# Optimization experiments

Hardware: AMD Instinct MI355X
Metric: run time of the kernel (lower is better)

The kernel has to match this reference:

```python
import jax, jax.numpy as jnp
import numpy as np
import math

EMB = 512

def setup_inputs() -> dict:
    key = jax.random.key(0)
    ks = jax.random.split(key, 7)
    B, L, E = 4, 4096, EMB
    s = 1.0 / math.sqrt(E)
    return {
        "x": jax.random.normal(ks[0], (B, L, E), dtype=jnp.float32),
        "Wq": jax.random.normal(ks[1], (E, E), dtype=jnp.float32) * s,
        "bq": jax.random.normal(ks[2], (E,), dtype=jnp.float32) * 0.01,
        "Wk": jax.random.normal(ks[3], (E, E), dtype=jnp.float32) * s,
        "bk": jax.random.normal(ks[4], (E,), dtype=jnp.float32) * 0.01,
        "Wv": jax.random.normal(ks[5], (E, E), dtype=jnp.float32) * s,
        "bv": jax.random.normal(ks[6], (E,), dtype=jnp.float32) * 0.01,
    }

def reference(x, Wq, bq, Wk, bk, Wv, bv):
    # x: [B, L, E]; Linear weights stored torch-style [out, in]
    E = x.shape[-1]
    L = x.shape[1]
    q = jnp.einsum('ble,fe->blf', x, Wq) + bq
    k = jnp.einsum('ble,fe->blf', x, Wk) + bk
    v = jnp.einsum('ble,fe->blf', x, Wv) + bv
    qk = jnp.einsum('bqe,bke->bqk', q, k)  # [B, L, L]
    # causal mask: strict upper triangle filled with -1e9 BEFORE scaling (as in source)
    mask = jnp.triu(jnp.ones((L, L), dtype=bool), k=1)
    qk = jnp.where(mask, jnp.float32(-1e9), qk)
    att = jax.nn.softmax(qk / jnp.sqrt(jnp.float32(E)), axis=-1)
    return jnp.einsum('bqk,bke->bqe', att, v)
```

## Files before the change

kernel.cpp:

```cpp
#include <hip/hip_runtime.h>

typedef unsigned short u16;
typedef unsigned int u32;
typedef short bf16x8 __attribute__((ext_vector_type(8)));
typedef float f32x4 __attribute__((ext_vector_type(4)));
typedef u16 u16x8 __attribute__((ext_vector_type(8)));
typedef u16 u16x4 __attribute__((ext_vector_type(4)));

typedef const __attribute__((address_space(1))) u32* gas_ptr;
typedef __attribute__((address_space(3))) u32* las_ptr;

#define LQ   4096
#define EMB  512
#define NB   4
#define MROWS (NB * LQ)
#define QSCALE 0.04419417382415922f

__device__ __forceinline__ u16 f2bf(float f) {
  unsigned u = __builtin_bit_cast(unsigned, f);
  u += 0x7fffu + ((u >> 16) & 1u);
  return (u16)(u >> 16);
}
__device__ __forceinline__ float bf2f(u16 h) {
  unsigned u = ((unsigned)h) << 16;
  return __builtin_bit_cast(float, u);
}

__global__ void prep_w(const float* __restrict__ Wq, const float* __restrict__ bq,
                       const float* __restrict__ Wk, const float* __restrict__ bk,
                       const float* __restrict__ Wv, const float* __restrict__ bv,
                       u16* __restrict__ wqb, u16* __restrict__ wkb, u16* __restrict__ wvb,
                       float* __restrict__ bias) {
  int i = blockIdx.x * 256 + threadIdx.x;
  if (i < EMB * EMB) {
    wqb[i] = f2bf(Wq[i] * QSCALE);
    wkb[i] = f2bf(Wk[i]);
    wvb[i] = f2bf(Wv[i]);
  }
  if (i < EMB) {
    bias[i]           = bq[i] * QSCALE;
    bias[EMB + i]     = bk[i];
    bias[2 * EMB + i] = bv[i];
  }
}

__global__ void prep_x(const float* __restrict__ x, u16* __restrict__ xb) {
  int i = blockIdx.x * 256 + threadIdx.x;
  const float4* p = (const float4*)(x + (size_t)i * 8);
  float4 a = p[0], b = p[1];
  u16x8 o;
  o[0] = f2bf(a.x); o[1] = f2bf(a.y); o[2] = f2bf(a.z); o[3] = f2bf(a.w);
  o[4] = f2bf(b.x); o[5] = f2bf(b.y); o[6] = f2bf(b.z); o[7] = f2bf(b.w);
  *(u16x8*)(xb + (size_t)i * 8) = o;
}

__device__ __forceinline__ void stage128_256t(const u16* g, int ld, u16* lds, int tid) {
  int wave = tid >> 6;
#pragma unroll
  for (int p = 0; p < 4; ++p) {
    int c = tid + p * 256;
    int row = c >> 3, hh = c & 7;
    int h = hh ^ (row & 7);
    const u16* src = g + (size_t)row * ld + h * 8;
    u16* dst = lds + wave * 512 + p * 2048;
    __builtin_amdgcn_global_load_lds((gas_ptr)(const void*)src, (las_ptr)(void*)dst, 16, 0, 0);
  }
}

__device__ __forceinline__ void gemm_core_db(
    const u16* __restrict__ A, int lda,
    const u16* __restrict__ B, int ldb,
    int kIters, u16* lds,
    f32x4 acc[4][4], int tid, int lane, int wr, int wc)
{
  stage128_256t(A, lda, lds, tid);
  stage128_256t(B, ldb, lds + 8192, tid);
  for (int kb = 0; kb < kIters; ++kb) {
    u16* ldsA = lds + (kb & 1) * 16384;
    u16* ldsB = ldsA + 8192;
    __syncthreads();
    if (kb + 1 < kIters) {
      u16* nA = lds + ((kb + 1) & 1) * 16384;
      stage128_256t(A + (kb + 1) * 64, lda, nA, tid);
      stage128_256t(B + (kb + 1) * 64, ldb, nA + 8192, tid);
    }
#pragma unroll
    for (int s = 0; s < 2; ++s) {
      bf16x8 af[4], bfr[4];
#pragma unroll
      for (int m = 0; m < 4; ++m) {
        int row = wr * 64 + m * 16 + (lane & 15);
        int hh = (s * 4 + (lane >> 4)) ^ (row & 7);
        af[m] = *(const bf16x8*)(ldsA + row * 64 + hh * 8);
      }
#pragma unroll
      for (int n = 0; n < 4; ++n) {
        int row = wc * 64 + n * 16 + (lane & 15);
        int hh = (s * 4 + (lane >> 4)) ^ (row & 7);
        bfr[n] = *(const bf16x8*)(ldsB + row * 64 + hh * 8);
      }
#pragma unroll
      for (int m = 0; m < 4; ++m)
#pragma unroll
        for (int n = 0; n < 4; ++n)
          acc[m][n] = __builtin_amdgcn_mfma_f32_16x16x32_bf16(af[m], bfr[n], acc[m][n], 0, 0, 0);
    }
  }
}

__global__ __launch_bounds__(256, 2) void k_qkv(
    const u16* __restrict__ xb,
    const u16* __restrict__ w0, const u16* __restrict__ w1, const u16* __restrict__ w2,
    const float* __restrict__ bias,
    u16* __restrict__ o0, u16* __restrict__ o1, u16* __restrict__ o2)
{
  __shared__ __align__(16) u16 lds[32768];
  int bi = blockIdx.x;
  int which = bi >> 9;
  int t = bi & 511;
  int rt = t >> 2, ct = t & 3;
  const u16* W = (which == 0) ? w0 : (which == 1) ? w1 : w2;
  const float* bs = bias + which * EMB;
  int tid = threadIdx.x, lane = tid & 63, wave = tid >> 6;
  int wr = wave >> 1, wc = wave & 1;
  f32x4 acc[4][4];
#pragma unroll
  for (int m = 0; m < 4; ++m)
#pragma unroll
    for (int n = 0; n < 4; ++n) acc[m][n] = (f32x4)0.0f;

  gemm_core_db(xb + (size_t)rt * 128 * EMB, EMB,
               W + (size_t)ct * 128 * EMB, EMB, EMB / 64,
               lds, acc, tid, lane, wr, wc);

#pragma unroll
  for (int m = 0; m < 4; ++m)
#pragma unroll
    for (int n = 0; n < 4; ++n) {
      int row0 = rt * 128 + wr * 64 + m * 16 + ((lane >> 4) << 2);
      int col  = ct * 128 + wc * 64 + n * 16 + (lane & 15);
      float bv = bs[col];
      if (which < 2) {
        u16* out = (which == 0) ? o0 : o1;
#pragma unroll
        for (int r = 0; r < 4; ++r)
          out[(size_t)(row0 + r) * EMB + col] = f2bf(acc[m][n][r] + bv);
      } else {
        int b = row0 >> 12, l0 = row0 & (LQ - 1);
        u16x4 pk;
#pragma unroll
        for (int r = 0; r < 4; ++r) pk[r] = f2bf(acc[m][n][r] + bv);
        *(u16x4*)(o2 + ((size_t)(b * EMB + col)) * LQ + l0) = pk;
      }
    }
}

__global__ __launch_bounds__(256, 2) void k_qk(
    const u16* __restrict__ Q, const u16* __restrict__ K,
    u16* __restrict__ S, int bstart)
{
  __shared__ __align__(16) u16 lds[32768];
  int t = blockIdx.x;
  int b_local = t / 528;
  int i = t - b_local * 528;
  int qi = (int)((sqrtf(8.f * (float)i + 1.f) - 1.f) * 0.5f);
  while ((qi + 1) * (qi + 2) / 2 <= i) ++qi;
  while (qi * (qi + 1) / 2 > i) --qi;
  int ki = i - qi * (qi + 1) / 2;
  int bg = bstart + b_local;

  int tid = threadIdx.x, lane = tid & 63, wave = tid >> 6;
  int wr = wave >> 1, wc = wave & 1;
  f32x4 acc[4][4];
#pragma unroll
  for (int m = 0; m < 4; ++m)
#pragma unroll
    for (int n = 0; n < 4; ++n) acc[m][n] = (f32x4)0.0f;

  gemm_core_db(Q + ((size_t)bg * LQ + qi * 128) * EMB, EMB,
               K + ((size_t)bg * LQ + ki * 128) * EMB, EMB, EMB / 64,
               lds, acc, tid, lane, wr, wc);

  u16* Sb = S + (size_t)b_local * LQ * LQ;
#pragma unroll
  for (int m = 0; m < 4; ++m)
#pragma unroll
    for (int n = 0; n < 4; ++n) {
      int row0 = qi * 128 + wr * 64 + m * 16 + ((lane >> 4) << 2);
      int col  = ki * 128 + wc * 64 + n * 16 + (lane & 15);
#pragma unroll
      for (int r = 0; r < 4; ++r) {
        int row = row0 + r;
        float v = (col > row) ? -1e9f : acc[m][n][r];
        Sb[(size_t)row * LQ + col] = f2bf(v);
      }
    }
}

__global__ __launch_bounds__(512, 1) void k_pv2(
    const u16* __restrict__ S, const u16* __restrict__ Vt,
    float* __restrict__ out, int bstart, int bcount)
{
  __shared__ __align__(16) u16 sA[4096];
  __shared__ __align__(16) u16 sB[65536];
  __shared__ __align__(16) u16 sP[2048];
  __shared__ float sF[32];
  __shared__ float sL[32];

  int bi = blockIdx.x;
  int pairidx = bi / bcount;
  int b_local = bi - pairidx * bcount;
  int bg = bstart + b_local;
  int rtA = pairidx, rtB = 127 - pairidx;
  int unitsA = (rtA + 2) >> 1;
  int total = unitsA + ((rtB + 2) >> 1);

  const u16* Sbase = S + (size_t)b_local * LQ * LQ;
  const u16* Vb = Vt + (size_t)bg * EMB * LQ;

  int tid = threadIdx.x, lane = tid & 63, wave = tid >> 6;
  int l15 = lane & 15, lhi = lane >> 4;
  int srow = tid >> 4;
  int scg  = tid & 15;
  int shh  = ((scg >> 1) ^ (srow & 7)) * 8 + (scg & 1) * 4;

  f32x4 acc[2][4];
#pragma unroll
  for (int m = 0; m < 2; ++m)
#pragma unroll
    for (int n = 0; n < 4; ++n) acc[m][n] = (f32x4)0.0f;
  float mrun = -3.0e38f, lrun = 0.f;

  auto stage_unit = [&](int i) {
    int ph = (i >= unitsA) ? 1 : 0;
    int rt = ph ? rtB : rtA;
    int k0 = (ph ? (i - unitsA) : i) * 64;
    const u16* ga = Sbase + (size_t)(rt * 32) * LQ + k0;
    const u16* gb = Vb + k0;
    u16* bA = sA + (i & 1) * 2048;
    u16* bB = sB + (i & 1) * 32768;
    if (wave < 4) {
      int ca = wave * 64 + lane;
      int row = ca >> 3, h = ca & 7;
      __builtin_amdgcn_global_load_lds(
          (gas_ptr)(const void*)(ga + (size_t)row * LQ + (h ^ (row & 7)) * 8),
          (las_ptr)(void*)(bA + wave * 512), 16, 0, 0);
    }
#pragma unroll
    for (int p = 0; p < 8; ++p) {
      int cb = wave * 512 + p * 64 + lane;
      int col = cb >> 3, h = cb & 7;
      __builtin_amdgcn_global_load_lds(
          (gas_ptr)(const void*)(gb + (size_t)col * LQ + (h ^ (col & 7)) * 8),
          (las_ptr)(void*)(bB + wave * 4096 + p * 512), 16, 0, 0);
    }
  };

  auto epilogue = [&](int rt) {
    if (scg == 0) sL[srow] = 1.0f / lrun;
    __syncthreads();
    float li[2][4];
#pragma unroll
    for (int m = 0; m < 2; ++m)
#pragma unroll
      for (int r = 0; r < 4; ++r) li[m][r] = sL[m * 16 + lhi * 4 + r];
#pragma unroll
    for (int m = 0; m < 2; ++m)
#pragma unroll
      for (int r = 0; r < 4; ++r) {
        int grow = rt * 32 + m * 16 + lhi * 4 + r;
#pragma unroll
        for (int n = 0; n < 4; ++n) {
          int col = wave * 64 + n * 16 + l15;
          out[((size_t)bg * LQ + grow) * EMB + col] = acc[m][n][r] * li[m][r];
        }
      }
#pragma unroll
    for (int m = 0; m < 2; ++m)
#pragma unroll
      for (int n = 0; n < 4; ++n) acc[m][n] = (f32x4)0.0f;
    mrun = -3.0e38f;
    lrun = 0.f;
  };

  stage_unit(0);

  for (int i = 0; i < total; ++i) {
    u16* bA = sA + (i & 1) * 2048;
    u16* bB = sB + (i & 1) * 32768;
    __syncthreads();
    if (i + 1 < total) stage_unit(i + 1);
    if (i == unitsA) epilogue(rtA);

    u16x4 raw = *(const u16x4*)(bA + srow * 64 + shh);
    float s0 = bf2f(raw[0]), s1 = bf2f(raw[1]), s2 = bf2f(raw[2]), s3 = bf2f(raw[3]);
    float tmax = fmaxf(fmaxf(s0, s1), fmaxf(s2, s3));
#pragma unroll
    for (int off = 1; off <= 8; off <<= 1) tmax = fmaxf(tmax, __shfl_xor(tmax, off));
    float mnew = (tmax > mrun + 8.f) ? tmax : mrun;
    float f = __expf(mrun - mnew);
    mrun = mnew;
    float e0 = __expf(s0 - mrun), e1 = __expf(s1 - mrun);
    float e2 = __expf(s2 - mrun), e3 = __expf(s3 - mrun);
    float rs = (e0 + e1) + (e2 + e3);
#pragma unroll
    for (int off = 1; off <= 8; off <<= 1) rs += __shfl_xor(rs, off);
    lrun = lrun * f + rs;
    u16x4 pk;
    pk[0] = f2bf(e0); pk[1] = f2bf(e1); pk[2] = f2bf(e2); pk[3] = f2bf(e3);
    *(u16x4*)(sP + srow * 64 + shh) = pk;
    if (scg == 0) sF[srow] = f;
    __syncthreads();

    float fr[2][4];
#pragma unroll
    for (int m = 0; m < 2; ++m)
#pragma unroll
      for (int r = 0; r < 4; ++r) fr[m][r] = sF[m * 16 + lhi * 4 + r];
#pragma unroll
    for (int m = 0; m < 2; ++m)
#pragma unroll
      for (int n = 0; n < 4; ++n)
#pragma unroll
        for (int r = 0; r < 4; ++r) acc[m][n][r] *= fr[m][r];

#pragma unroll
    for (int s = 0; s < 2; ++s) {
      bf16x8 af[2];
#pragma unroll
      for (int m = 0; m < 2; ++m) {
        int row = m * 16 + l15;
        int hh = (s * 4 + lhi) ^ (row & 7);
        af[m] = *(const bf16x8*)(sP + row * 64 + hh * 8);
      }
#pragma unroll
      for (int n = 0; n < 4; ++n) {
        int col = wave * 64 + n * 16 + l15;
        int hh = (s * 4 + lhi) ^ (col & 7);
        bf16x8 bv = *(const bf16x8*)(bB + col * 64 + hh * 8);
#pragma unroll
        for (int m = 0; m < 2; ++m)
          acc[m][n] = __builtin_amdgcn_mfma_f32_16x16x32_bf16(af[m], bv, acc[m][n], 0, 0, 0);
      }
    }
  }
  __syncthreads();
  epilogue(rtB);
}

extern "C" void kernel_launch(void* const* d_in, const int* in_sizes, int n_in,
                              void* d_out, int out_size, void* d_ws, size_t ws_size,
                              hipStream_t stream) {
  const float* x  = (const float*)d_in[0];
  const float* Wq = (const float*)d_in[1];
  const float* bq = (const float*)d_in[2];
  const float* Wk = (const float*)d_in[3];
  const float* bk = (const float*)d_in[4];
  const float* Wv = (const float*)d_in[5];
  const float* bv = (const float*)d_in[6];

  char* ws = (char*)d_ws;
  size_t off = 0;
  u16* xb  = (u16*)(ws + off); off += (size_t)MROWS * EMB * 2;
  u16* wqb = (u16*)(ws + off); off += (size_t)EMB * EMB * 2;
  u16* wkb = (u16*)(ws + off); off += (size_t)EMB * EMB * 2;
  u16* wvb = (u16*)(ws + off); off += (size_t)EMB * EMB * 2;
  float* bias = (float*)(ws + off); off += 3 * EMB * 4;
  off = (off + 255) & ~(size_t)255;
  u16* Qb  = (u16*)(ws + off); off += (size_t)MROWS * EMB * 2;
  u16* Kb  = (u16*)(ws + off); off += (size_t)MROWS * EMB * 2;
  u16* Vtb = (u16*)(ws + off); off += (size_t)MROWS * EMB * 2;
  size_t fixed = off;
  size_t s_full = (size_t)NB * LQ * LQ * 2;
  int bcap = (ws_size >= fixed + s_full) ? NB : 1;
  u16* Sb = (u16*)(ws + fixed);

  prep_w<<<(EMB * EMB + 255) / 256, 256, 0, stream>>>(Wq, bq, Wk, bk, Wv, bv,
                                                      wqb, wkb, wvb, bias);
  prep_x<<<(MROWS * EMB / 8) / 256, 256, 0, stream>>>(x, xb);

  k_qkv<<<1536, 256, 0, stream>>>(xb, wqb, wkb, wvb, bias, Qb, Kb, Vtb);

  for (int bs = 0; bs < NB; bs += bcap) {
    int bc = (bs + bcap <= NB) ? bcap : (NB - bs);
    k_qk<<<528 * bc, 256, 0, stream>>>(Qb, Kb, Sb, bs);
    k_pv2<<<64 * bc, 512, 0, stream>>>(Sb, Vtb, (float*)d_out, bs, bc);
  }
}
```

Measured before the change: 244.4 us.

## Restructure PV kernel to 128-row tiles with pipelined register softmax

Replaces the paired 32-row PV kernel with one that handles a 128-row query tile per block. Each V tile staged in LDS is now reused across 128 rows instead of 32. S rows are loaded into registers two steps ahead, and the softmax for the next step is computed while the current step's MFMAs run. Accumulator rescaling is skipped when no row's running max changed. The cost is fewer blocks (32 per batch) with uneven causal work per block, which risks load imbalance and lower occupancy from a large accumulator register footprint.

```diff
diff --git a/kernel.cpp b/kernel.cpp
--- a/kernel.cpp
+++ b/kernel.cpp
@@ -197,155 +197,172 @@
     }
 }
 
-__global__ __launch_bounds__(512, 1) void k_pv2(
+__global__ __launch_bounds__(512, 1) void k_pv3(
     const u16* __restrict__ S, const u16* __restrict__ Vt,
     float* __restrict__ out, int bstart, int bcount)
 {
-  __shared__ __align__(16) u16 sA[4096];
-  __shared__ __align__(16) u16 sB[65536];
-  __shared__ __align__(16) u16 sP[2048];
-  __shared__ float sF[32];
-  __shared__ float sL[32];
+  __shared__ __align__(16) u16 sV[65536];
+  __shared__ __align__(16) u16 sP[8192];
+  __shared__ float sF[128];
+  __shared__ float sL[128];
+  __shared__ int   sFlag[8];
 
   int bi = blockIdx.x;
-  int pairidx = bi / bcount;
-  int b_local = bi - pairidx * bcount;
+  int rt = bi / bcount;
+  int b_local = bi - rt * bcount;
   int bg = bstart + b_local;
-  int rtA = pairidx, rtB = 127 - pairidx;
-  int unitsA = (rtA + 2) >> 1;
-  int total = unitsA + ((rtB + 2) >> 1);
-
-  const u16* Sbase = S + (size_t)b_local * LQ * LQ;
+  int total = 2 * (rt + 1);
+
+  const u16* Sbase = S + ((size_t)b_local * LQ + rt * 128) * LQ;
   const u16* Vb = Vt + (size_t)bg * EMB * LQ;
 
   int tid = threadIdx.x, lane = tid & 63, wave = tid >> 6;
   int l15 = lane & 15, lhi = lane >> 4;
-  int srow = tid >> 4;
-  int scg  = tid & 15;
-  int shh  = ((scg >> 1) ^ (srow & 7)) * 8 + (scg & 1) * 4;
-
-  f32x4 acc[2][4];
-#pragma unroll
-  for (int m = 0; m < 2; ++m)
+  int r0 = tid >> 3;
+  int cc = tid & 7;
+
+  f32x4 acc[8][4];
+#pragma unroll
+  for (int m = 0; m < 8; ++m)
 #pragma unroll
     for (int n = 0; n < 4; ++n) acc[m][n] = (f32x4)0.0f;
-  float mrun = -3.0e38f, lrun = 0.f;
-
-  auto stage_unit = [&](int i) {
-    int ph = (i >= unitsA) ? 1 : 0;
-    int rt = ph ? rtB : rtA;
-    int k0 = (ph ? (i - unitsA) : i) * 64;
-    const u16* ga = Sbase + (size_t)(rt * 32) * LQ + k0;
-    const u16* gb = Vb + k0;
-    u16* bA = sA + (i & 1) * 2048;
-    u16* bB = sB + (i & 1) * 32768;
-    if (wave < 4) {
-      int ca = wave * 64 + lane;
-      int row = ca >> 3, h = ca & 7;
-      __builtin_amdgcn_global_load_lds(
-          (gas_ptr)(const void*)(ga + (size_t)row * LQ + (h ^ (row & 7)) * 8),
-          (las_ptr)(void*)(bA + wave * 512), 16, 0, 0);
-    }
+  float m0 = -3.0e38f, m1 = -3.0e38f, l0 = 0.f, l1 = 0.f;
+
+  auto stageV = [&](int i, u16* buf) {
+    const u16* gb = Vb + i * 64;
 #pragma unroll
     for (int p = 0; p < 8; ++p) {
       int cb = wave * 512 + p * 64 + lane;
-      int col = cb >> 3, h = cb & 7;
+      int col = cb >> 3, h = (cb & 7) ^ (col & 7);
       __builtin_amdgcn_global_load_lds(
-          (gas_ptr)(const void*)(gb + (size_t)col * LQ + (h ^ (col & 7)) * 8),
-          (las_ptr)(void*)(bB + wave * 4096 + p * 512), 16, 0, 0);
+          (gas_ptr)(const void*)(gb + (size_t)col * LQ + h * 8),
+          (las_ptr)(void*)(buf + wave * 4096 + p * 512), 16, 0, 0);
     }
   };
-
-  auto epilogue = [&](int rt) {
-    if (scg == 0) sL[srow] = 1.0f / lrun;
+  auto issueA = [&](int i, u16x8 (&ar)[2]) {
+    const u16* ga = Sbase + i * 64 + cc * 8;
+    ar[0] = *(const u16x8*)(ga + (size_t)r0 * LQ);
+    ar[1] = *(const u16x8*)(ga + (size_t)(r0 + 64) * LQ);
+  };
+  auto softmax = [&](u16x8 (&ar)[2], u16x8& pf0, u16x8& pf1, float& fo0, float& fo1) {
+    float s0[8], s1[8];
+#pragma unroll
+    for (int j = 0; j < 8; ++j) { s0[j] = bf2f(ar[0][j]); s1[j] = bf2f(ar[1][j]); }
+    float mx0 = fmaxf(fmaxf(fmaxf(s0[0], s0[1]), fmaxf(s0[2], s0[3])),
+                      fmaxf(fmaxf(s0[4], s0[5]), fmaxf(s0[6], s0[7])));
+    float mx1 = fmaxf(fmaxf(fmaxf(s1[0], s1[1]), fmaxf(s1[2], s1[3])),
+                      fmaxf(fmaxf(s1[4], s1[5]), fmaxf(s1[6], s1[7])));
+#pragma unroll
+    for (int off = 1; off <= 4; off <<= 1) {
+      mx0 = fmaxf(mx0, __shfl_xor(mx0, off));
+      mx1 = fmaxf(mx1, __shfl_xor(mx1, off));
+    }
+    float mn0 = (mx0 > m0 + 8.f) ? mx0 : m0;
+    float mn1 = (mx1 > m1 + 8.f) ? mx1 : m1;
+    float f0 = __expf(m0 - mn0);
+    float f1 = __expf(m1 - mn1);
+    m0 = mn0; m1 = mn1;
+    float t0 = 0.f, t1 = 0.f;
+#pragma unroll
+    for (int j = 0; j < 8; ++j) {
+      float e0 = __expf(s0[j] - m0);
+      float e1 = __expf(s1[j] - m1);
+      t0 += e0; t1 += e1;
+      pf0[j] = f2bf(e0); pf1[j] = f2bf(e1);
+    }
+#pragma unroll
+    for (int off = 1; off <= 4; off <<= 1) {
+      t0 += __shfl_xor(t0, off);
+      t1 += __shfl_xor(t1, off);
+    }
+    l0 = l0 * f0 + t0;
+    l1 = l1 * f1 + t1;
+    fo0 = f0; fo1 = f1;
+  };
+
+  u16x8 ar0[2], ar1[2];
+  issueA(0, ar0);
+  stageV(0, sV);
+  issueA(1, ar1);
+  {
+    u16x8 pf0, pf1; float f0s, f1s;
+    softmax(ar0, pf0, pf1, f0s, f1s);
+    int hh = cc ^ (r0 & 7);
+    *(u16x8*)(sP + r0 * 64 + hh * 8) = pf0;
+    *(u16x8*)(sP + (r0 + 64) * 64 + hh * 8) = pf1;
+    if (cc == 0) { sF[r0] = f0s; sF[r0 + 64] = f1s; }
+    int fl = __any((f0s < 1.f) || (f1s < 1.f)) ? 1 : 0;
+    if (lane == 0) sFlag[wave] = fl;
+  }
+
+  auto body = [&](int i, u16x8 (&cur)[2], u16x8 (&nxt)[2], u16* vb, u16* vbN) {
     __syncthreads();
-    float li[2][4];
-#pragma unroll
-    for (int m = 0; m < 2; ++m)
-#pragma unroll
-      for (int r = 0; r < 4; ++r) li[m][r] = sL[m * 16 + lhi * 4 + r];
-#pragma unroll
-    for (int m = 0; m < 2; ++m)
-#pragma unroll
-      for (int r = 0; r < 4; ++r) {
-        int grow = rt * 32 + m * 16 + lhi * 4 + r;
-#pragma unroll
-        for (int n = 0; n < 4; ++n) {
-          int col = wave * 64 + n * 16 + l15;
-          out[((size_t)bg * LQ + grow) * EMB + col] = acc[m][n][r] * li[m][r];
-        }
-      }
-#pragma unroll
-    for (int m = 0; m < 2; ++m)
-#pragma unroll
-      for (int n = 0; n < 4; ++n) acc[m][n] = (f32x4)0.0f;
-    mrun = -3.0e38f;
-    lrun = 0.f;
-  };
-
-  stage_unit(0);
-
-  for (int i = 0; i < total; ++i) {
-    u16* bA = sA + (i & 1) * 2048;
-    u16* bB = sB + (i & 1) * 32768;
-    __syncthreads();
-    if (i + 1 < total) stage_unit(i + 1);
-    if (i == unitsA) epilogue(rtA);
-
-    u16x4 raw = *(const u16x4*)(bA + srow * 64 + shh);
-    float s0 = bf2f(raw[0]), s1 = bf2f(raw[1]), s2 = bf2f(raw[2]), s3 = bf2f(raw[3]);
-    float tmax = fmaxf(fmaxf(s0, s1), fmaxf(s2, s3));
-#pragma unroll
-    for (int off = 1; off <= 8; off <<= 1) tmax = fmaxf(tmax, __shfl_xor(tmax, off));
-    float mnew = (tmax > mrun + 8.f) ? tmax : mrun;
-    float f = __expf(mrun - mnew);
-    mrun = mnew;
-    float e0 = __expf(s0 - mrun), e1 = __expf(s1 - mrun);
-    float e2 = __expf(s2 - mrun), e3 = __expf(s3 - mrun);
-    float rs = (e0 + e1) + (e2 + e3);
-#pragma unroll
-    for (int off = 1; off <= 8; off <<= 1) rs += __shfl_xor(rs, off);
-    lrun = lrun * f + rs;
-    u16x4 pk;
-    pk[0] = f2bf(e0); pk[1] = f2bf(e1); pk[2] = f2bf(e2); pk[3] = f2bf(e3);
-    *(u16x4*)(sP + srow * 64 + shh) = pk;
-    if (scg == 0) sF[srow] = f;
-    __syncthreads();
-
-    float fr[2][4];
-#pragma unroll
-    for (int m = 0; m < 2; ++m)
-#pragma unroll
-      for (int r = 0; r < 4; ++r) fr[m][r] = sF[m * 16 + lhi * 4 + r];
-#pragma unroll
-    for (int m = 0; m < 2; ++m)
-#pragma unroll
-      for (int n = 0; n < 4; ++n)
-#pragma unroll
-        for (int r = 0; r < 4; ++r) acc[m][n][r] *= fr[m][r];
-
+    bool have = (i + 1 < total);
+    if (have) stageV(i + 1, vbN);
+    if (i + 2 < total) issueA(i + 2, cur);
+    int4 fA = *(const int4*)&sFlag[0];
+    int4 fB = *(const int4*)&sFlag[4];
+    if (fA.x | fA.y | fA.z | fA.w | fB.x | fB.y | fB.z | fB.w) {
+#pragma unroll
+      for (int m = 0; m < 8; ++m) {
+        f32x4 sf = *(const f32x4*)&sF[m * 16 + lhi * 4];
+#pragma unroll
+        for (int n = 0; n < 4; ++n)
+#pragma unroll
+          for (int r = 0; r < 4; ++r) acc[m][n][r] *= sf[r];
+      }
+    }
+    u16x8 pf0, pf1; float f0s = 1.f, f1s = 1.f;
+    if (have) softmax(nxt, pf0, pf1, f0s, f1s);
 #pragma unroll
     for (int s = 0; s < 2; ++s) {
-      bf16x8 af[2];
-#pragma unroll
-      for (int m = 0; m < 2; ++m) {
-        int row = m * 16 + l15;
-        int hh = (s * 4 + lhi) ^ (row & 7);
-        af[m] = *(const bf16x8*)(sP + row * 64 + hh * 8);
-      }
+      bf16x8 bv[4];
 #pragma unroll
       for (int n = 0; n < 4; ++n) {
         int col = wave * 64 + n * 16 + l15;
-        int hh = (s * 4 + lhi) ^ (col & 7);
-        bf16x8 bv = *(const bf16x8*)(bB + col * 64 + hh * 8);
-#pragma unroll
-        for (int m = 0; m < 2; ++m)
-          acc[m][n] = __builtin_amdgcn_mfma_f32_16x16x32_bf16(af[m], bv, acc[m][n], 0, 0, 0);
-      }
-    }
-  }
+        bv[n] = *(const bf16x8*)(vb + col * 64 + ((s * 4 + lhi) ^ (col & 7)) * 8);
+      }
+#pragma unroll
+      for (int m = 0; m < 8; ++m) {
+        int row = m * 16 + l15;
+        bf16x8 pa = *(const bf16x8*)(sP + row * 64 + ((s * 4 + lhi) ^ (row & 7)) * 8);
+#pragma unroll
+        for (int n = 0; n < 4; ++n)
+          acc[m][n] = __builtin_amdgcn_mfma_f32_16x16x32_bf16(pa, bv[n], acc[m][n], 0, 0, 0);
+      }
+    }
+    __syncthreads();
+    if (have) {
+      int hh = cc ^ (r0 & 7);
+      *(u16x8*)(sP + r0 * 64 + hh * 8) = pf0;
+      *(u16x8*)(sP + (r0 + 64) * 64 + hh * 8) = pf1;
+      if (cc == 0) { sF[r0] = f0s; sF[r0 + 64] = f1s; }
+      int fl = __any((f0s < 1.f) || (f1s < 1.f)) ? 1 : 0;
+      if (lane == 0) sFlag[wave] = fl;
+    }
+  };
+
+  int half = total >> 1;
+  for (int h = 0; h < half; ++h) {
+    body(2 * h,     ar0, ar1, sV,         sV + 32768);
+    body(2 * h + 1, ar1, ar0, sV + 32768, sV);
+  }
+
+  if (cc == 0) { sL[r0] = 1.0f / l0; sL[r0 + 64] = 1.0f / l1; }
   __syncthreads();
-  epilogue(rtB);
+#pragma unroll
+  for (int m = 0; m < 8; ++m) {
+    f32x4 li = *(const f32x4*)&sL[m * 16 + lhi * 4];
+#pragma unroll
+    for (int r = 0; r < 4; ++r) {
+      int grow = rt * 128 + m * 16 + lhi * 4 + r;
+#pragma unroll
+      for (int n = 0; n < 4; ++n) {
+        int col = wave * 64 + n * 16 + l15;
+        out[((size_t)bg * LQ + grow) * EMB + col] = acc[m][n][r] * li[r];
+      }
+    }
+  }
 }
 
 extern "C" void kernel_launch(void* const* d_in, const int* in_sizes, int n_in,
@@ -384,6 +401,6 @@
   for (int bs = 0; bs < NB; bs += bcap) {
     int bc = (bs + bcap <= NB) ? bcap : (NB - bs);
     k_qk<<<528 * bc, 256, 0, stream>>>(Qb, Kb, Sb, bs);
-    k_pv2<<<64 * bc, 512, 0, stream>>>(Sb, Vtb, (float*)d_out, bs, bc);
-  }
-}
+    k_pv3<<<32 * bc, 512, 0, stream>>>(Sb, Vtb, (float*)d_out, bs, bc);
+  }
+}
```

Result: slower. 438.6 us (+79.4%).
